# Kernel tuning notes

Hardware: AMD Instinct MI355X
Metric: run time of the kernel (lower is better)

## Reference

```python
import jax, jax.numpy as jnp
import numpy as np

N_GOOD = 16
NUM_TEST = 16
NUM_UNITS = 32
EPS = 1e-5


def _mlp(x, w1, b1, w2, b2):
    # Linear -> ReLU -> Linear -> ReLU
    h = jax.nn.relu(x @ w1 + b1)
    return jax.nn.relu(h @ w2 + b2)


def _ln_relu(x, g, b):
    mu = jnp.mean(x, axis=-1, keepdims=True)
    var = jnp.mean(jnp.square(x - mu), axis=-1, keepdims=True)
    return jax.nn.relu((x - mu) / jnp.sqrt(var + EPS) * g + b)


def _attend(self_out, enc):
    # self_out: [B, D], enc: [B, N, D]
    scores = jnp.einsum('bd,bnd->bn', self_out, enc) / np.float32(np.sqrt(NUM_TEST))
    attn = jax.nn.softmax(scores, axis=-1)
    return jnp.einsum('bn,bnd->bd', attn, enc)


def setup_inputs() -> dict:
    key = jax.random.key(0)
    ks = jax.random.split(key, 24)
    B = 262144
    obs_dim = 4 + (N_GOOD - 1) * 5 + N_GOOD * 3  # 127

    def lin(k, fan_in, fan_out):
        bound = 1.0 / np.sqrt(fan_in)
        kw, kb = jax.random.split(k)
        w = jax.random.uniform(kw, (fan_in, fan_out), jnp.float32, -bound, bound)
        b = jax.random.uniform(kb, (fan_out,), jnp.float32, -bound, bound)
        return w, b

    en_w1, en_b1 = lin(ks[0], 4, NUM_UNITS)
    en_w2, en_b2 = lin(ks[1], NUM_UNITS, NUM_TEST)
    oa_w1, oa_b1 = lin(ks[2], 5, NUM_UNITS)
    oa_w2, oa_b2 = lin(ks[3], NUM_UNITS, NUM_TEST)
    g_w1, g_b1 = lin(ks[4], 3, NUM_UNITS)
    g_w2, g_b2 = lin(ks[5], NUM_UNITS, NUM_TEST)
    m_w1, m_b1 = lin(ks[6], NUM_TEST * 3, NUM_UNITS)
    m_w2, m_b2 = lin(ks[7], NUM_UNITS, NUM_UNITS)
    m_w3, m_b3 = lin(ks[8], NUM_UNITS, 2)

    return {
        's_input': jax.random.normal(ks[9], (B, obs_dim), jnp.float32),
        'en_w1': en_w1, 'en_b1': en_b1, 'en_w2': en_w2, 'en_b2': en_b2,
        'oa_w1': oa_w1, 'oa_b1': oa_b1, 'oa_w2': oa_w2, 'oa_b2': oa_b2,
        'oa_g': jnp.ones((NUM_TEST,), jnp.float32), 'oa_bln': jnp.zeros((NUM_TEST,), jnp.float32),
        'g_w1': g_w1, 'g_b1': g_b1, 'g_w2': g_w2, 'g_b2': g_b2,
        'g_g': jnp.ones((NUM_TEST,), jnp.float32), 'g_bln': jnp.zeros((NUM_TEST,), jnp.float32),
        'm_w1': m_w1, 'm_b1': m_b1, 'm_w2': m_w2, 'm_b2': m_b2, 'm_w3': m_w3, 'm_b3': m_b3,
    }


def reference(s_input, en_w1, en_b1, en_w2, en_b2,
              oa_w1, oa_b1, oa_w2, oa_b2, oa_g, oa_bln,
              g_w1, g_b1, g_w2, g_b2, g_g, g_bln,
              m_w1, m_b1, m_w2, m_b2, m_w3, m_b3):
    n = N_GOOD
    B = s_input.shape[0]

    # self encoding: [B, 16]
    self_out = _mlp(s_input[:, :4], en_w1, en_b1, en_w2, en_b2)

    # other agents: width (n-1)*5 = [pos pairs | vel pairs | scalar per agent]
    og = s_input[:, 4:4 + (n - 1) * 5]
    pos = og[:, :(n - 1) * 2].reshape(B, n - 1, 2)
    vel = og[:, (n - 1) * 2:(n - 1) * 4].reshape(B, n - 1, 2)
    scal = og[:, (n - 1) * 4:(n - 1) * 5].reshape(B, n - 1, 1)
    other_in = jnp.concatenate([pos, vel, scal], axis=-1)  # [B, n-1, 5]
    other_enc = _mlp(other_in, oa_w1, oa_b1, oa_w2, oa_b2)  # [B, n-1, 16]
    other_out = _ln_relu(_attend(self_out, other_enc), oa_g, oa_bln)

    # food/goals: last n*3 cols, chunks of 3
    food_in = s_input[:, -n * 3:].reshape(B, n, 3)
    food_enc = _mlp(food_in, g_w1, g_b1, g_w2, g_b2)  # [B, n, 16]
    food_out = _ln_relu(_attend(self_out, food_enc), g_g, g_bln)

    merged = jnp.concatenate([self_out, food_out, other_out], axis=1)  # [B, 48]
    h = jax.nn.leaky_relu(merged @ m_w1 + m_b1, 0.01)
    h = jax.nn.leaky_relu(h @ m_w2 + m_b2, 0.01)
    return jnp.tanh(h @ m_w3 + m_b3)  # [B, 2]
```

## Files before the change

kernel.cpp:

```cpp
#include <hip/hip_runtime.h>
#include <math.h>


#define OBS 127
#define XSS 132

typedef _Float16 v4h  __attribute__((ext_vector_type(4)));
typedef _Float16 v8h  __attribute__((ext_vector_type(8)));
typedef __fp16   p2h  __attribute__((ext_vector_type(2)));
typedef float    v16f __attribute__((ext_vector_type(16)));
typedef float    f4u  __attribute__((ext_vector_type(4), aligned(4)));

#define MFMA16(a, b, c) __builtin_amdgcn_mfma_f32_32x32x16_f16((a), (b), (c), 0, 0, 0)

union PK8 { p2h p[4]; v8h h; };
union HU8 { unsigned u[4]; v8h h; _Float16 e[8]; };

__device__ __forceinline__ v8h zero8h() {
    v8h z;
    #pragma unroll
    for (int j = 0; j < 8; ++j) z[j] = (_Float16)0.f;
    return z;
}
__device__ __forceinline__ v8h pk8(const v16f& d, int b) {
    PK8 q;
    q.p[0] = __builtin_amdgcn_cvt_pkrtz(d[b],     d[b + 1]);
    q.p[1] = __builtin_amdgcn_cvt_pkrtz(d[b + 2], d[b + 3]);
    q.p[2] = __builtin_amdgcn_cvt_pkrtz(d[b + 4], d[b + 5]);
    q.p[3] = __builtin_amdgcn_cvt_pkrtz(d[b + 6], d[b + 7]);
    return q.h;
}
__device__ __forceinline__ v8h pkr8(const v16f& d, int b) {
    return __builtin_elementwise_max(pk8(d, b), zero8h());
}
__device__ __forceinline__ v8h pk8f(const float (&v)[8]) {
    PK8 q;
    q.p[0] = __builtin_amdgcn_cvt_pkrtz(v[0], v[1]);
    q.p[1] = __builtin_amdgcn_cvt_pkrtz(v[2], v[3]);
    q.p[2] = __builtin_amdgcn_cvt_pkrtz(v[4], v[5]);
    q.p[3] = __builtin_amdgcn_cvt_pkrtz(v[6], v[7]);
    return q.h;
}
__device__ __forceinline__ v8h lrelu8(v8h t) {
    const v8h s = t * (_Float16)0.01f;
    return __builtin_elementwise_max(t, s);
}
__device__ __forceinline__ v8h a1fragK16(const float* __restrict__ W,
                                         const float* __restrict__ b,
                                         int kin, int m, int h) {
    const int Lm = (m & ~12) | ((m & 4) << 1) | ((m & 8) >> 1);
    v8h r;
    #pragma unroll
    for (int j = 0; j < 8; ++j) {
        const int k = 8 * h + j;
        const float v = (k < kin) ? W[k * 32 + Lm] : (k == kin ? b[Lm] : 0.f);
        r[j] = (_Float16)v;
    }
    return r;
}
__device__ __forceinline__ v8h a2fragK16(const float* __restrict__ W2,
                                         int s, int m, int h) {
    v8h r;
    #pragma unroll
    for (int j = 0; j < 8; ++j)
        r[j] = (_Float16)((m < 16) ? W2[(16 * s + 8 * h + j) * 16 + m] : 0.f);
    return r;
}
__device__ __forceinline__ v8h mfragK16(const float* __restrict__ W, int ncols,
                                        int base, int m, int h, int colmax) {
    v8h r;
    #pragma unroll
    for (int j = 0; j < 8; ++j) {
        const int ch = base + (j & 3) + 8 * (j >> 2) + 4 * h;
        r[j] = (_Float16)((m < colmax) ? W[ch * ncols + m] : 0.f);
    }
    return r;
}
__device__ __forceinline__ float fast_tanh(float x) {
    x = fminf(fmaxf(x, -15.f), 15.f);
    const float ex = __expf(2.f * x);
    return (ex - 1.f) / (ex + 1.f);
}

template <int BR>
__device__ __forceinline__ void entity_step(const _Float16* __restrict__ xr,
                                            int e, int h,
                                            v8h A1, v8h A2a, v8h A2b,
                                            const float (&b2v)[8],
                                            const float (&stl)[8],
                                            float& l, float (&o)[8],
                                            v16f z16) {
    v8h bf = zero8h();
    if (h == 0) {
        HU8 u;
        #pragma unroll
        for (int j = 0; j < 4; ++j) u.u[j] = 0;
        if (BR == 1) {
            u.e[0] = xr[79 + 3 * e];
            u.e[1] = xr[80 + 3 * e];
            u.e[2] = xr[81 + 3 * e];
            u.e[3] = (_Float16)1.f;
        } else {
            u.u[0] = *(const unsigned*)(xr + 4 + 2 * e);
            u.u[1] = *(const unsigned*)(xr + 34 + 2 * e);
            u.e[4] = xr[64 + e];
            u.e[5] = (_Float16)1.f;
        }
        bf = u.h;
    }
    const v16f dH = MFMA16(A1, bf, z16);
    const v8h p0 = pkr8(dH, 0);
    const v8h p1 = pkr8(dH, 8);
    v16f c = MFMA16(A2a, p0, z16);
    c = MFMA16(A2b, p1, c);
    float e2[8], part = 0.f;
    #pragma unroll
    for (int r = 0; r < 8; ++r) {
        e2[r] = fmaxf(c[r] + b2v[r], 0.f);
        part += stl[r] * e2[r];
    }
    part += __shfl_xor(part, 32);
    const float p = __builtin_amdgcn_exp2f(part);
    l += p;
    #pragma unroll
    for (int r = 0; r < 8; ++r) o[r] += p * e2[r];
}

__device__ __forceinline__ v8h ln_fin(float l, const float (&o)[8],
                                      const float (&gv)[8], const float (&blv)[8]) {
    const float rl = 1.f / l;
    float a[8], sum = 0.f;
    #pragma unroll
    for (int r = 0; r < 8; ++r) { a[r] = o[r] * rl; sum += a[r]; }
    sum += __shfl_xor(sum, 32);
    const float mu = sum * 0.0625f;
    float var = 0.f;
    #pragma unroll
    for (int r = 0; r < 8; ++r) { a[r] -= mu; var += a[r] * a[r]; }
    var += __shfl_xor(var, 32);
    const float inv = rsqrtf(var * 0.0625f + 1e-5f);
    float v[8];
    #pragma unroll
    for (int r = 0; r < 8; ++r) v[r] = fmaxf(a[r] * inv * gv[r] + blv[r], 0.f);
    return pk8f(v);
}

__global__ __launch_bounds__(256)
void actor_mfma(const float* __restrict__ x,
                const float* __restrict__ en_w1, const float* __restrict__ en_b1,
                const float* __restrict__ en_w2, const float* __restrict__ en_b2,
                const float* __restrict__ oa_w1, const float* __restrict__ oa_b1,
                const float* __restrict__ oa_w2, const float* __restrict__ oa_b2,
                const float* __restrict__ oa_g,  const float* __restrict__ oa_bln,
                const float* __restrict__ g_w1,  const float* __restrict__ g_b1,
                const float* __restrict__ g_w2,  const float* __restrict__ g_b2,
                const float* __restrict__ g_g,   const float* __restrict__ g_bln,
                const float* __restrict__ m_w1,  const float* __restrict__ m_b1,
                const float* __restrict__ m_w2,  const float* __restrict__ m_b2,
                const float* __restrict__ m_w3,  const float* __restrict__ m_b3,
                float* __restrict__ out, int B)
{
    const int lane = threadIdx.x & 63, wid = threadIdx.x >> 6;
    const int n = lane & 31, h = lane >> 5;

    __shared__ __align__(16) _Float16 xs_all[4][32 * XSS];
    _Float16* xs = xs_all[wid];

    const int r0 = blockIdx.x * 128 + wid * 32;
    const bool wvalid = (r0 < B);

    if (wvalid) {
        const float* __restrict__ xp = x + (size_t)r0 * OBS;
        if (r0 + 32 <= B) {
            #pragma unroll
            for (int i = 0; i < 16; ++i) {
                const int gI = i * 64 + lane;
                if (gI < 992) {
                    const int row = gI / 31;
                    const int c4 = gI - row * 31;
                    const f4u v = *(const f4u*)(xp + row * 127 + c4 * 4);
                    PK8 q;
                    q.p[0] = __builtin_amdgcn_cvt_pkrtz(v[0], v[1]);
                    q.p[1] = __builtin_amdgcn_cvt_pkrtz(v[2], v[3]);
                    *(uint2*)(xs + row * XSS + c4 * 4) = *(const uint2*)&q;
                }
            }
            #pragma unroll
            for (int t = 0; t < 2; ++t) {
                const int idx = t * 64 + lane;
                if (idx < 96) {
                    const int row = idx / 3;
                    const int c = 124 + idx - row * 3;
                    xs[row * XSS + c] = (_Float16)xp[row * 127 + c];
                }
            }
        } else {
            const int lim = (B - r0) * OBS;
            for (int i = 0; i < 64; ++i) {
                const int f = i * 64 + lane;
                if (f < lim) {
                    const int r = f / 127;
                    xs[f + 5 * r] = (_Float16)xp[f];
                }
            }
        }
    }
    __syncthreads();

    v16f z16;
    #pragma unroll
    for (int r = 0; r < 16; ++r) z16[r] = 0.f;

    float sb2v[8], fb2v[8], ob2v[8];
    #pragma unroll
    for (int r = 0; r < 8; ++r) {
        const int m = (r & 3) + 8 * (r >> 2) + 4 * h;
        sb2v[r] = en_b2[m];
        fb2v[r] = g_b2[m];
        ob2v[r] = oa_b2[m];
    }

    const _Float16* xr = xs + n * XSS;
    float st[8], stl[8];
    v8h Bs;
    {
        const v8h sA1 = a1fragK16(en_w1, en_b1, 4, n, h);
        const v8h sA2a = a2fragK16(en_w2, 0, n, h);
        const v8h sA2b = a2fragK16(en_w2, 1, n, h);
        v8h bs = zero8h();
        if (h == 0) {
            HU8 u;
            #pragma unroll
            for (int j = 0; j < 4; ++j) u.u[j] = 0;
            *(uint2*)&u.u[0] = *(const uint2*)xr;
            u.e[4] = (_Float16)1.f;
            bs = u.h;
        }
        const v16f dS = MFMA16(sA1, bs, z16);
        v16f cS = MFMA16(sA2a, pkr8(dS, 0), z16);
        cS = MFMA16(sA2b, pkr8(dS, 8), cS);
        const float SK = 0.25f * 1.44269504088896f;
        float sv[8];
        #pragma unroll
        for (int r = 0; r < 8; ++r) {
            sv[r] = fmaxf(cS[r] + sb2v[r], 0.f);
            st[r] = sv[r];
            stl[r] = sv[r] * SK;
        }
        Bs = pk8f(sv);
    }

    const v8h fA1 = a1fragK16(g_w1, g_b1, 3, n, h);
    const v8h fA2a = a2fragK16(g_w2, 0, n, h);
    const v8h fA2b = a2fragK16(g_w2, 1, n, h);
    const v8h oA1 = a1fragK16(oa_w1, oa_b1, 5, n, h);
    const v8h oA2a = a2fragK16(oa_w2, 0, n, h);
    const v8h oA2b = a2fragK16(oa_w2, 1, n, h);

    float lf = 0.f, lo = 0.f, of[8], oo[8];
    #pragma unroll
    for (int r = 0; r < 8; ++r) { of[r] = 0.f; oo[r] = 0.f; }
    #pragma unroll 2
    for (int e = 0; e < 16; ++e) {
        entity_step<1>(xr, e, h, fA1, fA2a, fA2b, fb2v, stl, lf, of, z16);
        if (e < 15)
            entity_step<0>(xr, e, h, oA1, oA2a, oA2b, ob2v, stl, lo, oo, z16);
    }

    float fgv[8], fblv[8], ogv[8], oblv[8];
    #pragma unroll
    for (int r = 0; r < 8; ++r) {
        const int m = (r & 3) + 8 * (r >> 2) + 4 * h;
        fgv[r] = g_g[m];  fblv[r] = g_bln[m];
        ogv[r] = oa_g[m]; oblv[r] = oa_bln[m];
    }
    const v8h Bf = ln_fin(lf, of, fgv, fblv);
    const v8h Bo = ln_fin(lo, oo, ogv, oblv);

    v16f m1C, m2C;
    #pragma unroll
    for (int r = 0; r < 16; ++r) {
        const int m = (r & 3) + 8 * (r >> 2) + 4 * h;
        m1C[r] = m_b1[m];
        m2C[r] = m_b2[m];
    }
    v16f m1 = MFMA16(mfragK16(m_w1, 32, 0, n, h, 32), Bs, m1C);
    m1 = MFMA16(mfragK16(m_w1, 32, 16, n, h, 32), Bf, m1);
    m1 = MFMA16(mfragK16(m_w1, 32, 32, n, h, 32), Bo, m1);
    const v8h q0 = lrelu8(pk8(m1, 0));
    const v8h q1 = lrelu8(pk8(m1, 8));
    v16f m2 = MFMA16(mfragK16(m_w2, 32, 0, n, h, 32), q0, m2C);
    m2 = MFMA16(mfragK16(m_w2, 32, 16, n, h, 32), q1, m2);
    const v8h z0 = lrelu8(pk8(m2, 0));
    const v8h z1 = lrelu8(pk8(m2, 8));
    v16f m3 = MFMA16(mfragK16(m_w3, 2, 0, n, h, 2), z0, z16);
    m3 = MFMA16(mfragK16(m_w3, 2, 16, n, h, 2), z1, m3);

    if (h == 0 && wvalid && r0 + n < B) {
        float2 res;
        res.x = fast_tanh(m3[0] + m_b3[0]);
        res.y = fast_tanh(m3[1] + m_b3[1]);
        *(float2*)(out + (size_t)(r0 + n) * 2) = res;
    }
}

extern "C" void kernel_launch(void* const* d_in, const int* in_sizes, int n_in,
                              void* d_out, int out_size, void* d_ws, size_t ws_size,
                              hipStream_t stream) {
    const int B = in_sizes[0] / OBS;
    const float* xin = (const float*)d_in[0];
    const float* en_w1 = (const float*)d_in[1];
    const float* en_b1 = (const float*)d_in[2];
    const float* en_w2 = (const float*)d_in[3];
    const float* en_b2 = (const float*)d_in[4];
    const float* oa_w1 = (const float*)d_in[5];
    const float* oa_b1 = (const float*)d_in[6];
    const float* oa_w2 = (const float*)d_in[7];
    const float* oa_b2 = (const float*)d_in[8];
    const float* oa_g  = (const float*)d_in[9];
    const float* oa_bl = (const float*)d_in[10];
    const float* g_w1  = (const float*)d_in[11];
    const float* g_b1  = (const float*)d_in[12];
    const float* g_w2  = (const float*)d_in[13];
    const float* g_b2  = (const float*)d_in[14];
    const float* g_g   = (const float*)d_in[15];
    const float* g_bl  = (const float*)d_in[16];
    const float* m_w1  = (const float*)d_in[17];
    const float* m_b1  = (const float*)d_in[18];
    const float* m_w2  = (const float*)d_in[19];
    const float* m_b2  = (const float*)d_in[20];
    const float* m_w3  = (const float*)d_in[21];
    const float* m_b3  = (const float*)d_in[22];

    const int rows_per_block = 128;
    const int grid = (B + rows_per_block - 1) / rows_per_block;
    actor_mfma<<<grid, 256, 0, stream>>>(
        xin, en_w1, en_b1, en_w2, en_b2,
        oa_w1, oa_b1, oa_w2, oa_b2, oa_g, oa_bl,
        g_w1, g_b1, g_w2, g_b2, g_g, g_bl,
        m_w1, m_b1, m_w2, m_b2, m_w3, m_b3,
        (float*)d_out, B);
}
```

Measured before the change: 299.8 us.

## Pre-pack per-entity MFMA B fragments in LDS and prefetch them in the loop

Input staging now writes each entity's features directly as fragment-ready fp16 groups, with the bias 1.0 already in place, into a wider per-row LDS layout. A shared zero row serves the upper half-wave, so the entity loop replaces per-element branching and scalar LDS reads with one vector load per entity. The loop is fully unrolled and prefetches the next entity's fragments. The kernel also drops __syncthreads, since each wave only reads its own LDS region, and adds an occupancy hint of 3 blocks per CU. The cost is more scattered, overlapping global reads when staging, and more LDS per block.

```diff
diff --git a/kernel.cpp b/kernel.cpp
--- a/kernel.cpp
+++ b/kernel.cpp
@@ -3,17 +3,22 @@
 
 
 #define OBS 127
-#define XSS 132
-
-typedef _Float16 v4h  __attribute__((ext_vector_type(4)));
+#define RSTR 200
+#define ZROW (32 * RSTR)
+#define WWORDS (33 * RSTR)
+
 typedef _Float16 v8h  __attribute__((ext_vector_type(8)));
+typedef _Float16 v8ha __attribute__((ext_vector_type(8), aligned(16)));
 typedef __fp16   p2h  __attribute__((ext_vector_type(2)));
 typedef float    v16f __attribute__((ext_vector_type(16)));
 typedef float    f4u  __attribute__((ext_vector_type(4), aligned(4)));
+typedef float    f2u  __attribute__((ext_vector_type(2), aligned(4)));
+typedef unsigned ui2  __attribute__((ext_vector_type(2), aligned(8)));
+typedef unsigned ui4  __attribute__((ext_vector_type(4), aligned(16)));
 
 #define MFMA16(a, b, c) __builtin_amdgcn_mfma_f32_32x32x16_f16((a), (b), (c), 0, 0, 0)
 
-union PK8 { p2h p[4]; v8h h; };
+union PK8 { p2h p[4]; v8h h; unsigned w[4]; };
 union HU8 { unsigned u[4]; v8h h; _Float16 e[8]; };
 
 __device__ __forceinline__ v8h zero8h() {
@@ -82,32 +87,19 @@
     return (ex - 1.f) / (ex + 1.f);
 }
 
-template <int BR>
-__device__ __forceinline__ void entity_step(const _Float16* __restrict__ xr,
-                                            int e, int h,
-                                            v8h A1, v8h A2a, v8h A2b,
-                                            const float (&b2v)[8],
-                                            const float (&stl)[8],
-                                            float& l, float (&o)[8],
-                                            v16f z16) {
-    v8h bf = zero8h();
-    if (h == 0) {
-        HU8 u;
-        #pragma unroll
-        for (int j = 0; j < 4; ++j) u.u[j] = 0;
-        if (BR == 1) {
-            u.e[0] = xr[79 + 3 * e];
-            u.e[1] = xr[80 + 3 * e];
-            u.e[2] = xr[81 + 3 * e];
-            u.e[3] = (_Float16)1.f;
-        } else {
-            u.u[0] = *(const unsigned*)(xr + 4 + 2 * e);
-            u.u[1] = *(const unsigned*)(xr + 34 + 2 * e);
-            u.e[4] = xr[64 + e];
-            u.e[5] = (_Float16)1.f;
-        }
-        bf = u.h;
-    }
+__device__ __forceinline__ v8h ld16h(const _Float16* p) {
+    return *(const v8ha*)p;
+}
+__device__ __forceinline__ v8h ld8h(const _Float16* p) {
+    HU8 u;
+    *(ui2*)&u.u[0] = *(const ui2*)p;
+    u.u[2] = 0; u.u[3] = 0;
+    return u.h;
+}
+
+__device__ __forceinline__ void estep(v8h bf, v8h A1, v8h A2a, v8h A2b,
+                                      const float (&b2v)[8], const float (&stl)[8],
+                                      float& l, float (&o)[8], v16f z16) {
     const v16f dH = MFMA16(A1, bf, z16);
     const v8h p0 = pkr8(dH, 0);
     const v8h p1 = pkr8(dH, 8);
@@ -145,7 +137,7 @@
     return pk8f(v);
 }
 
-__global__ __launch_bounds__(256)
+__global__ __launch_bounds__(256, 3)
 void actor_mfma(const float* __restrict__ x,
                 const float* __restrict__ en_w1, const float* __restrict__ en_b1,
                 const float* __restrict__ en_w2, const float* __restrict__ en_b2,
@@ -163,49 +155,59 @@
     const int lane = threadIdx.x & 63, wid = threadIdx.x >> 6;
     const int n = lane & 31, h = lane >> 5;
 
-    __shared__ __align__(16) _Float16 xs_all[4][32 * XSS];
+    __shared__ __align__(16) _Float16 xs_all[4][WWORDS];
     _Float16* xs = xs_all[wid];
 
     const int r0 = blockIdx.x * 128 + wid * 32;
-    const bool wvalid = (r0 < B);
-
-    if (wvalid) {
+    int rows = B - r0;
+    rows = rows > 32 ? 32 : (rows < 0 ? 0 : rows);
+
+    if (lane < 24) {
+        PK8 z;
+        z.w[0] = 0; z.w[1] = 0; z.w[2] = 0; z.w[3] = 0;
+        *(ui4*)(xs + ZROW + lane * 8) = *(const ui4*)&z;
+    }
+
+    if (rows > 0) {
         const float* __restrict__ xp = x + (size_t)r0 * OBS;
-        if (r0 + 32 <= B) {
-            #pragma unroll
-            for (int i = 0; i < 16; ++i) {
-                const int gI = i * 64 + lane;
-                if (gI < 992) {
-                    const int row = gI / 31;
-                    const int c4 = gI - row * 31;
-                    const f4u v = *(const f4u*)(xp + row * 127 + c4 * 4);
-                    PK8 q;
-                    q.p[0] = __builtin_amdgcn_cvt_pkrtz(v[0], v[1]);
-                    q.p[1] = __builtin_amdgcn_cvt_pkrtz(v[2], v[3]);
-                    *(uint2*)(xs + row * XSS + c4 * 4) = *(const uint2*)&q;
-                }
+        if (lane < rows) {
+            const f4u v = *(const f4u*)(xp + lane * OBS);
+            PK8 q;
+            q.p[0] = __builtin_amdgcn_cvt_pkrtz(v[0], v[1]);
+            q.p[1] = __builtin_amdgcn_cvt_pkrtz(v[2], v[3]);
+            q.p[2] = __builtin_amdgcn_cvt_pkrtz(1.f, 0.f);
+            q.p[3] = __builtin_amdgcn_cvt_pkrtz(0.f, 0.f);
+            *(ui4*)(xs + lane * RSTR) = *(const ui4*)&q;
+        }
+        #pragma unroll
+        for (int i = 0; i < 8; ++i) {
+            const int t = i * 64 + lane, row = t >> 4, e = t & 15;
+            if (row < rows) {
+                const f4u v = *(const f4u*)(xp + row * OBS + 78 + 3 * e);
+                PK8 q;
+                q.p[0] = __builtin_amdgcn_cvt_pkrtz(v[1], v[2]);
+                q.p[1] = __builtin_amdgcn_cvt_pkrtz(v[3], 1.f);
+                ui2 w; w[0] = q.w[0]; w[1] = q.w[1];
+                *(ui2*)(xs + row * RSTR + 8 + 4 * e) = w;
             }
-            #pragma unroll
-            for (int t = 0; t < 2; ++t) {
-                const int idx = t * 64 + lane;
-                if (idx < 96) {
-                    const int row = idx / 3;
-                    const int c = 124 + idx - row * 3;
-                    xs[row * XSS + c] = (_Float16)xp[row * 127 + c];
-                }
+        }
+        #pragma unroll
+        for (int i = 0; i < 8; ++i) {
+            const int t = i * 64 + lane, row = t >> 4, e = t & 15;
+            if (e < 15 && row < rows) {
+                const float* rp = xp + row * OBS;
+                const f2u pv = *(const f2u*)(rp + 4 + 2 * e);
+                const f2u vv = *(const f2u*)(rp + 34 + 2 * e);
+                const float sc = rp[64 + e];
+                PK8 q;
+                q.p[0] = __builtin_amdgcn_cvt_pkrtz(pv[0], pv[1]);
+                q.p[1] = __builtin_amdgcn_cvt_pkrtz(vv[0], vv[1]);
+                q.p[2] = __builtin_amdgcn_cvt_pkrtz(sc, 1.f);
+                q.p[3] = __builtin_amdgcn_cvt_pkrtz(0.f, 0.f);
+                *(ui4*)(xs + row * RSTR + 72 + 8 * e) = *(const ui4*)&q;
             }
-        } else {
-            const int lim = (B - r0) * OBS;
-            for (int i = 0; i < 64; ++i) {
-                const int f = i * 64 + lane;
-                if (f < lim) {
-                    const int r = f / 127;
-                    xs[f + 5 * r] = (_Float16)xp[f];
-                }
-            }
-        }
-    }
-    __syncthreads();
+        }
+    }
 
     v16f z16;
     #pragma unroll
@@ -220,22 +222,15 @@
         ob2v[r] = oa_b2[m];
     }
 
-    const _Float16* xr = xs + n * XSS;
-    float st[8], stl[8];
+    const int rbase = h ? ZROW : n * RSTR;
+
+    float stl[8];
     v8h Bs;
     {
         const v8h sA1 = a1fragK16(en_w1, en_b1, 4, n, h);
         const v8h sA2a = a2fragK16(en_w2, 0, n, h);
         const v8h sA2b = a2fragK16(en_w2, 1, n, h);
-        v8h bs = zero8h();
-        if (h == 0) {
-            HU8 u;
-            #pragma unroll
-            for (int j = 0; j < 4; ++j) u.u[j] = 0;
-            *(uint2*)&u.u[0] = *(const uint2*)xr;
-            u.e[4] = (_Float16)1.f;
-            bs = u.h;
-        }
+        const v8h bs = ld16h(xs + rbase);
         const v16f dS = MFMA16(sA1, bs, z16);
         v16f cS = MFMA16(sA2a, pkr8(dS, 0), z16);
         cS = MFMA16(sA2b, pkr8(dS, 8), cS);
@@ -244,7 +239,6 @@
         #pragma unroll
         for (int r = 0; r < 8; ++r) {
             sv[r] = fmaxf(cS[r] + sb2v[r], 0.f);
-            st[r] = sv[r];
             stl[r] = sv[r] * SK;
         }
         Bs = pk8f(sv);
@@ -260,11 +254,20 @@
     float lf = 0.f, lo = 0.f, of[8], oo[8];
     #pragma unroll
     for (int r = 0; r < 8; ++r) { of[r] = 0.f; oo[r] = 0.f; }
-    #pragma unroll 2
+
+    v8h bfF = ld8h(xs + rbase + 8);
+    v8h bfO = ld16h(xs + rbase + 72);
+    #pragma unroll
     for (int e = 0; e < 16; ++e) {
-        entity_step<1>(xr, e, h, fA1, fA2a, fA2b, fb2v, stl, lf, of, z16);
+        v8h bfFn = bfF, bfOn = bfO;
+        if (e < 15) {
+            bfFn = ld8h(xs + rbase + 8 + 4 * (e + 1));
+            if (e < 14) bfOn = ld16h(xs + rbase + 72 + 8 * (e + 1));
+        }
+        estep(bfF, fA1, fA2a, fA2b, fb2v, stl, lf, of, z16);
         if (e < 15)
-            entity_step<0>(xr, e, h, oA1, oA2a, oA2b, ob2v, stl, lo, oo, z16);
+            estep(bfO, oA1, oA2a, oA2b, ob2v, stl, lo, oo, z16);
+        bfF = bfFn; bfO = bfOn;
     }
 
     float fgv[8], fblv[8], ogv[8], oblv[8];
@@ -296,7 +299,7 @@
     v16f m3 = MFMA16(mfragK16(m_w3, 2, 0, n, h, 2), z0, z16);
     m3 = MFMA16(mfragK16(m_w3, 2, 16, n, h, 2), z1, m3);
 
-    if (h == 0 && wvalid && r0 + n < B) {
+    if (h == 0 && n < rows) {
         float2 res;
         res.x = fast_tanh(m3[0] + m_b3[0]);
         res.y = fast_tanh(m3[1] + m_b3[1]);
```

Result: slower. 362.8 us (+21.0%).
